# Kernel tuning notes

Measured on AMD Instinct MI355X. Metric: run time of the kernel, lower is better.

Reference implementation:

```python
import math
import jax, jax.numpy as jnp
import numpy as np

B, L, F, H = 16, 1024, 512, 8
D = F // H
FACTOR = 5.0
KEEP_MINLEN = 15.0


def setup_inputs() -> dict:
    key = jax.random.key(0)
    ks = jax.random.split(key, 12)
    inp = {
        "query": jax.random.normal(ks[0], (B, L, F), jnp.float32),
        "key": jax.random.normal(ks[1], (B, L, F), jnp.float32),
        "value": jax.random.normal(ks[2], (B, L, F), jnp.float32),
        "mask": jnp.ones((B, 1, L), jnp.int32),
    }
    s = 0.02
    inp["Wq"] = jax.random.normal(ks[3], (F, F), jnp.float32) * s
    inp["bq"] = jnp.zeros((F,), jnp.float32)
    inp["Wk"] = jax.random.normal(ks[4], (F, F), jnp.float32) * s
    inp["bk"] = jnp.zeros((F,), jnp.float32)
    inp["Wv"] = jax.random.normal(ks[5], (F, F), jnp.float32) * s
    inp["bv"] = jnp.zeros((F,), jnp.float32)
    inp["Wo"] = jax.random.normal(ks[6], (F, F), jnp.float32) * s
    inp["bo"] = jnp.zeros((F,), jnp.float32)
    return inp


def _n_top(Lq: int) -> int:
    if Lq <= KEEP_MINLEN:
        return Lq
    u = int(round(FACTOR * math.ceil(math.log(Lq))))
    return min(u, Lq)


def reference(query, key, value, mask, Wq, bq, Wk, bk, Wv, bv, Wo, bo):
    def proj(x, W, b):
        # torch nn.Linear: x @ W.T + b ; then (B,L,H,D) -> (B,H,L,D)
        return (x @ W.T + b).reshape(B, L, H, D).transpose(0, 2, 1, 3)

    q = proj(query, Wq, bq)
    k = proj(key, Wk, bk)
    v = proj(value, Wv, bv)

    # prob_QK with index=None: full (unscaled) QK to compute sparsity measure M
    scores_full = jnp.einsum('bhqd,bhkd->bhqk', q, k)  # (B,H,L,L)
    M = scores_full.max(-1) - scores_full.mean(-1)      # (B,H,L)
    u = _n_top(L)
    _, idx = jax.lax.top_k(M, u)                        # (B,H,u)

    q_red = jnp.take_along_axis(q, idx[..., None], axis=2)  # (B,H,u,D)
    scores = jnp.einsum('bhud,bhkd->bhuk', q_red, k) / math.sqrt(D)

    neg = (mask == 0)[:, None, :, :]  # (B,1,1,L) broadcasts over heads/queries
    scores = jnp.where(neg, -jnp.inf, scores)
    attn = jax.nn.softmax(scores, axis=-1)
    attn = jnp.where(neg, 0.0, attn)

    ctx_top = jnp.einsum('bhuk,bhkd->bhud', attn, v)   # (B,H,u,D)

    # initial context = mean of V over keys, broadcast to all queries
    context = jnp.broadcast_to(v.mean(axis=2, keepdims=True), (B, H, L, D))
    bi = jnp.arange(B)[:, None, None]
    hi = jnp.arange(H)[None, :, None]
    context = context.at[bi, hi, idx].set(ctx_top)

    x = context.transpose(0, 2, 1, 3).reshape(B, L, H * D)
    return x @ Wo.T + bo
```

## Files before the change

### kernel.cpp

```cpp
#include <hip/hip_runtime.h>
#include <math.h>

#define B_ 16
#define L_ 1024
#define H_ 8
#define U_ 35

typedef float f32x4 __attribute__((ext_vector_type(4)));
typedef short bf16x8 __attribute__((ext_vector_type(8)));

__device__ __forceinline__ unsigned short f2bf(float x) {
    unsigned int u = __float_as_uint(x);
    u += 0x7FFFu + ((u >> 16) & 1u);
    return (unsigned short)(u >> 16);
}
__device__ __forceinline__ float bf2f(unsigned short b) {
    return __uint_as_float(((unsigned int)b) << 16);
}

#define MFMA(a, b, c) __builtin_amdgcn_mfma_f32_16x16x32_bf16((a), (b), (c), 0, 0, 0)

#define OFF_V      ((size_t)0)
#define OFF_QHI    ((size_t)8388608)
#define OFF_QLO    ((size_t)12582912)
#define OFF_X      OFF_QHI
#define OFF_CTXP   OFF_QHI
#define OFF_KHI    ((size_t)16777216)
#define OFF_KLO    ((size_t)20971520)
#define OFF_S      ((size_t)25165824)
#define OFF_WQH    OFF_S
#define OFF_WQL    ((size_t)(OFF_S + 131072))
#define OFF_WKH    ((size_t)(OFF_S + 262144))
#define OFF_WKL    ((size_t)(OFF_S + 393216))
#define OFF_WVH    ((size_t)(OFF_S + 524288))
#define OFF_WVL    ((size_t)(OFF_S + 655360))
#define OFF_M      ((size_t)29753344)
#define OFF_KMEAN  ((size_t)29884416)
#define OFF_VMEAN  ((size_t)29892608)
#define OFF_CTX    ((size_t)29900800)
#define OFF_IDX    ((size_t)30187520)
#define OFF_WOH    ((size_t)30192000)
#define OFF_WOL    ((size_t)30323072)

__global__ __launch_bounds__(256) void split_w_kernel(
    const float* __restrict__ W, unsigned short* __restrict__ hi,
    unsigned short* __restrict__ lo)
{
    int i = blockIdx.x * 256 + threadIdx.x;
    float x = W[i];
    unsigned short h = f2bf(x);
    hi[i] = h;
    lo[i] = f2bf(x - bf2f(h));
}

__global__ __launch_bounds__(256) void gemm_mfma(
    const float* __restrict__ A,
    const unsigned short* __restrict__ Whi, const unsigned short* __restrict__ Wlo,
    const float* __restrict__ bias,
    float* __restrict__ outf,
    unsigned short* __restrict__ ohi, unsigned short* __restrict__ olo,
    const int head_layout)
{
    __shared__ unsigned short Ah[128][40];
    __shared__ unsigned short Al[128][40];
    __shared__ unsigned short Bh[128][40];
    __shared__ unsigned short Bl[128][40];
    const int tid = threadIdx.x, lane = tid & 63, wave = tid >> 6;
    const int m0 = blockIdx.x * 128, n0 = blockIdx.y * 128;
    const int wm = (wave >> 1) * 64, wn = (wave & 1) * 64;

    f32x4 zero4 = {0.f, 0.f, 0.f, 0.f};
    f32x4 acc[4][4];
#pragma unroll
    for (int i = 0; i < 4; i++)
#pragma unroll
        for (int j = 0; j < 4; j++) acc[i][j] = zero4;

    const int ar = tid >> 3, ac = (tid & 7) * 4;
    const int br = tid >> 2, bc = (tid & 3) * 8;
    const int kc = (lane >> 4) * 8;
    const int fr = lane & 15;

    for (int k0 = 0; k0 < 512; k0 += 32) {
        if (k0) __syncthreads();
#pragma unroll
        for (int p = 0; p < 4; ++p) {
            float4 a4 = *(const float4*)(A + (size_t)(m0 + ar + p * 32) * 512 + k0 + ac);
            ushort4 h4, l4;
            h4.x = f2bf(a4.x); l4.x = f2bf(a4.x - bf2f(h4.x));
            h4.y = f2bf(a4.y); l4.y = f2bf(a4.y - bf2f(h4.y));
            h4.z = f2bf(a4.z); l4.z = f2bf(a4.z - bf2f(h4.z));
            h4.w = f2bf(a4.w); l4.w = f2bf(a4.w - bf2f(h4.w));
            *(ushort4*)&Ah[ar + p * 32][ac] = h4;
            *(ushort4*)&Al[ar + p * 32][ac] = l4;
        }
#pragma unroll
        for (int p = 0; p < 2; ++p) {
            size_t off = (size_t)(n0 + br + p * 64) * 512 + k0 + bc;
            *(uint4*)&Bh[br + p * 64][bc] = *(const uint4*)(Whi + off);
            *(uint4*)&Bl[br + p * 64][bc] = *(const uint4*)(Wlo + off);
        }
        __syncthreads();

        bf16x8 ah[4], al[4];
#pragma unroll
        for (int mi = 0; mi < 4; ++mi) {
            int row = wm + mi * 16 + fr;
            ah[mi] = *(bf16x8*)&Ah[row][kc];
            al[mi] = *(bf16x8*)&Al[row][kc];
        }
#pragma unroll
        for (int ni = 0; ni < 4; ++ni) {
            int rn = wn + ni * 16 + fr;
            bf16x8 bh8 = *(bf16x8*)&Bh[rn][kc];
            bf16x8 bl8 = *(bf16x8*)&Bl[rn][kc];
#pragma unroll
            for (int mi = 0; mi < 4; ++mi) {
                acc[mi][ni] = MFMA(ah[mi], bh8, acc[mi][ni]);
                acc[mi][ni] = MFMA(ah[mi], bl8, acc[mi][ni]);
                acc[mi][ni] = MFMA(al[mi], bh8, acc[mi][ni]);
            }
        }
    }

    const int col = lane & 15, rq = (lane >> 4) * 4;
#pragma unroll
    for (int ni = 0; ni < 4; ++ni) {
        int n = n0 + wn + ni * 16 + col;
        float bn = bias[n];
#pragma unroll
        for (int mi = 0; mi < 4; ++mi) {
#pragma unroll
            for (int r = 0; r < 4; ++r) {
                int m = m0 + wm + mi * 16 + rq + r;
                float val = acc[mi][ni][r] + bn;
                if (head_layout) {
                    size_t off = ((size_t)((m >> 10) * H_ + (n >> 6)) * L_ + (m & 1023)) * 64 + (n & 63);
                    if (outf) outf[off] = val;
                    if (ohi) {
                        unsigned short h = f2bf(val);
                        ohi[off] = h;
                        olo[off] = f2bf(val - bf2f(h));
                    }
                } else {
                    outf[(size_t)m * 512 + n] = val;
                }
            }
        }
    }
}

__global__ __launch_bounds__(256) void mean_over_L(
    const float* __restrict__ src, float* __restrict__ dst)
{
    const int bh = blockIdx.x;
    const int d = threadIdx.x & 63, g = threadIdx.x >> 6;
    const float* p = src + ((size_t)bh * L_ + g * 256) * 64 + d;
    float s = 0.f;
#pragma unroll 8
    for (int l = 0; l < 256; l++) s += p[(size_t)l * 64];
    __shared__ float red[4][64];
    red[g][d] = s;
    __syncthreads();
    if (threadIdx.x < 64) {
        const int dd = threadIdx.x;
        dst[(size_t)bh * 64 + dd] =
            (red[0][dd] + red[1][dd] + red[2][dd] + red[3][dd]) * (1.0f / 1024.0f);
    }
}

__global__ __launch_bounds__(256) void mean_over_L_bf(
    const unsigned short* __restrict__ hi, const unsigned short* __restrict__ lo,
    float* __restrict__ dst)
{
    const int bh = blockIdx.x;
    const int d = threadIdx.x & 63, g = threadIdx.x >> 6;
    size_t base = ((size_t)bh * L_ + g * 256) * 64 + d;
    float s = 0.f;
#pragma unroll 8
    for (int l = 0; l < 256; l++) {
        size_t o = base + (size_t)l * 64;
        s += bf2f(hi[o]) + bf2f(lo[o]);
    }
    __shared__ float red[4][64];
    red[g][d] = s;
    __syncthreads();
    if (threadIdx.x < 64) {
        const int dd = threadIdx.x;
        dst[(size_t)bh * 64 + dd] =
            (red[0][dd] + red[1][dd] + red[2][dd] + red[3][dd]) * (1.0f / 1024.0f);
    }
}

__global__ __launch_bounds__(256) void qk_rowmax_mfma(
    const unsigned short* __restrict__ qhi, const unsigned short* __restrict__ qlo,
    const unsigned short* __restrict__ khi, const unsigned short* __restrict__ klo,
    const float* __restrict__ kmean, float* __restrict__ Mout)
{
    __shared__ unsigned short Qh[64][72], Ql[64][72];
    __shared__ unsigned short Kh[128][72], Kl[128][72];
    __shared__ float Mred[64][4];
    __shared__ float km[64];
    const int bh = blockIdx.y, q0 = blockIdx.x * 64;
    const int tid = threadIdx.x, lane = tid & 63, wave = tid >> 6;

    if (tid < 64) km[tid] = kmean[bh * 64 + tid];
    {
        int r = tid >> 2, c = (tid & 3) * 16;
        size_t off = ((size_t)bh * L_ + q0 + r) * 64 + c;
        *(uint4*)&Qh[r][c]     = *(const uint4*)(qhi + off);
        *(uint4*)&Qh[r][c + 8] = *(const uint4*)(qhi + off + 8);
        *(uint4*)&Ql[r][c]     = *(const uint4*)(qlo + off);
        *(uint4*)&Ql[r][c + 8] = *(const uint4*)(qlo + off + 8);
    }

    float rmax[4][4];
#pragma unroll
    for (int mi = 0; mi < 4; ++mi)
#pragma unroll
        for (int r = 0; r < 4; ++r) rmax[mi][r] = -INFINITY;

    const size_t kb = (size_t)bh * L_ * 64;
    const int sr = tid >> 2, sc = (tid & 3) * 16;
    const int fr = lane & 15;
    f32x4 zero4 = {0.f, 0.f, 0.f, 0.f};

    for (int kt = 0; kt < 8; ++kt) {
        __syncthreads();
        {
            size_t off = kb + (size_t)(kt * 128 + sr) * 64 + sc;
            *(uint4*)&Kh[sr][sc]          = *(const uint4*)(khi + off);
            *(uint4*)&Kh[sr][sc + 8]      = *(const uint4*)(khi + off + 8);
            *(uint4*)&Kl[sr][sc]          = *(const uint4*)(klo + off);
            *(uint4*)&Kl[sr][sc + 8]      = *(const uint4*)(klo + off + 8);
            size_t off2 = off + 64 * 64;
            *(uint4*)&Kh[sr + 64][sc]     = *(const uint4*)(khi + off2);
            *(uint4*)&Kh[sr + 64][sc + 8] = *(const uint4*)(khi + off2 + 8);
            *(uint4*)&Kl[sr + 64][sc]     = *(const uint4*)(klo + off2);
            *(uint4*)&Kl[sr + 64][sc + 8] = *(const uint4*)(klo + off2 + 8);
        }
        __syncthreads();

        f32x4 acc[4][2];
#pragma unroll
        for (int mi = 0; mi < 4; ++mi) { acc[mi][0] = zero4; acc[mi][1] = zero4; }

#pragma unroll
        for (int ks = 0; ks < 2; ++ks) {
            int kcol = ks * 32 + (lane >> 4) * 8;
            bf16x8 ah[4], al[4];
#pragma unroll
            for (int mi = 0; mi < 4; ++mi) {
                int row = mi * 16 + fr;
                ah[mi] = *(bf16x8*)&Qh[row][kcol];
                al[mi] = *(bf16x8*)&Ql[row][kcol];
            }
#pragma unroll
            for (int ni = 0; ni < 2; ++ni) {
                int krow = wave * 32 + ni * 16 + fr;
                bf16x8 bh8 = *(bf16x8*)&Kh[krow][kcol];
                bf16x8 bl8 = *(bf16x8*)&Kl[krow][kcol];
#pragma unroll
                for (int mi = 0; mi < 4; ++mi) {
                    acc[mi][ni] = MFMA(ah[mi], bh8, acc[mi][ni]);
                    acc[mi][ni] = MFMA(ah[mi], bl8, acc[mi][ni]);
                    acc[mi][ni] = MFMA(al[mi], bh8, acc[mi][ni]);
                }
            }
        }
#pragma unroll
        for (int mi = 0; mi < 4; ++mi)
#pragma unroll
            for (int r = 0; r < 4; ++r)
                rmax[mi][r] = fmaxf(rmax[mi][r], fmaxf(acc[mi][0][r], acc[mi][1][r]));
    }

#pragma unroll
    for (int mi = 0; mi < 4; ++mi)
#pragma unroll
        for (int r = 0; r < 4; ++r) {
            float v = rmax[mi][r];
            v = fmaxf(v, __shfl_xor(v, 1));
            v = fmaxf(v, __shfl_xor(v, 2));
            v = fmaxf(v, __shfl_xor(v, 4));
            v = fmaxf(v, __shfl_xor(v, 8));
            rmax[mi][r] = v;
        }
    if ((lane & 15) == 0) {
        int quad = lane >> 4;
#pragma unroll
        for (int mi = 0; mi < 4; ++mi)
#pragma unroll
            for (int r = 0; r < 4; ++r)
                Mred[mi * 16 + quad * 4 + r][wave] = rmax[mi][r];
    }
    __syncthreads();
    if (tid < 64) {
        float mx = fmaxf(fmaxf(Mred[tid][0], Mred[tid][1]),
                         fmaxf(Mred[tid][2], Mred[tid][3]));
        float dot = 0.f;
#pragma unroll 4
        for (int d = 0; d < 64; ++d)
            dot = fmaf(bf2f(Qh[tid][d]) + bf2f(Ql[tid][d]), km[d], dot);
        Mout[(size_t)bh * L_ + q0 + tid] = mx - dot;
    }
}

__global__ __launch_bounds__(256) void topk35(
    const float* __restrict__ Min, int* __restrict__ idx_out)
{
    const int bh = blockIdx.x;
    const int tid = threadIdx.x;
    __shared__ float vals[1024];
    __shared__ float wv[4];
    __shared__ int wi[4];
    for (int i = tid; i < 1024; i += 256) vals[i] = Min[(size_t)bh * 1024 + i];
    __syncthreads();
    for (int it = 0; it < U_; ++it) {
        float bv = -INFINITY; int bi = 1 << 30;
        for (int i = tid; i < 1024; i += 256) {
            float x = vals[i];
            if (x > bv) { bv = x; bi = i; }
        }
#pragma unroll
        for (int off = 32; off; off >>= 1) {
            float ov = __shfl_down(bv, off);
            int   oi = __shfl_down(bi, off);
            if (ov > bv || (ov == bv && oi < bi)) { bv = ov; bi = oi; }
        }
        if ((tid & 63) == 0) { wv[tid >> 6] = bv; wi[tid >> 6] = bi; }
        __syncthreads();
        if (tid == 0) {
#pragma unroll
            for (int w = 1; w < 4; ++w) {
                if (wv[w] > bv || (wv[w] == bv && wi[w] < bi)) { bv = wv[w]; bi = wi[w]; }
            }
            idx_out[bh * U_ + it] = bi;
            vals[bi] = -INFINITY;
        }
        __syncthreads();
    }
}

__global__ __launch_bounds__(256) void scores_red(
    const unsigned short* __restrict__ qhi, const unsigned short* __restrict__ qlo,
    const unsigned short* __restrict__ khi, const unsigned short* __restrict__ klo,
    const int* __restrict__ idx, const int* __restrict__ mask,
    float* __restrict__ S)
{
    __shared__ float Qs[64][36];
    __shared__ float Ks[64][68];
    const int bh = blockIdx.x;
    const int b = bh >> 3;
    const int tid = threadIdx.x;
    const int tk = tid & 63, tg = tid >> 6;

    for (int t = tid; t < 36 * 64; t += 256) {
        int u = t >> 6, d = t & 63;
        float val = 0.f;
        if (u < U_) {
            int l = idx[bh * U_ + u];
            size_t off = ((size_t)bh * L_ + l) * 64 + d;
            val = bf2f(qhi[off]) + bf2f(qlo[off]);
        }
        Qs[d][u] = val;
    }

    const size_t kb = (size_t)bh * L_ * 64;
    const int sr = tid >> 2, sc = (tid & 3) * 16;
    float acc[9];
    const int kt0 = blockIdx.y * 2;
    for (int ki = 0; ki < 2; ++ki) {
        int kt = kt0 + ki;
        if (ki) __syncthreads();
        {
            size_t off = kb + (size_t)(kt * 64 + sr) * 64 + sc;
            uint4 h0 = *(const uint4*)(khi + off);
            uint4 h1 = *(const uint4*)(khi + off + 8);
            uint4 l0 = *(const uint4*)(klo + off);
            uint4 l1 = *(const uint4*)(klo + off + 8);
            unsigned short hv[16], lv[16];
            *(uint4*)hv = h0; *(uint4*)(hv + 8) = h1;
            *(uint4*)lv = l0; *(uint4*)(lv + 8) = l1;
#pragma unroll
            for (int i = 0; i < 16; ++i)
                Ks[sc + i][sr] = bf2f(hv[i]) + bf2f(lv[i]);
        }
        __syncthreads();
#pragma unroll
        for (int j = 0; j < 9; j++) acc[j] = 0.f;
#pragma unroll 4
        for (int d = 0; d < 64; ++d) {
            float kv = Ks[d][tk];
#pragma unroll
            for (int j = 0; j < 9; j++) acc[j] = fmaf(Qs[d][tg + 4 * j], kv, acc[j]);
        }
        const int kcol = kt * 64 + tk;
        const bool msk = (mask[b * L_ + kcol] == 0);
#pragma unroll
        for (int j = 0; j < 9; j++) {
            int u = tg + 4 * j;
            if (u < U_)
                S[((size_t)bh * U_ + u) * 1024 + kcol] = msk ? -INFINITY : acc[j] * 0.125f;
        }
    }
}

__global__ __launch_bounds__(256) void softmax_rows(float* __restrict__ S)
{
    const size_t base = (size_t)blockIdx.x * 1024;
    const int tid = threadIdx.x;
    __shared__ float redm[4];
    __shared__ float reds[4];
    float4 v = *(const float4*)(S + base + tid * 4);
    float mx = fmaxf(fmaxf(v.x, v.y), fmaxf(v.z, v.w));
#pragma unroll
    for (int off = 32; off; off >>= 1) mx = fmaxf(mx, __shfl_down(mx, off));
    if ((tid & 63) == 0) redm[tid >> 6] = mx;
    __syncthreads();
    mx = fmaxf(fmaxf(redm[0], redm[1]), fmaxf(redm[2], redm[3]));
    float e0 = __expf(v.x - mx), e1 = __expf(v.y - mx);
    float e2 = __expf(v.z - mx), e3 = __expf(v.w - mx);
    float s = e0 + e1 + e2 + e3;
#pragma unroll
    for (int off = 32; off; off >>= 1) s += __shfl_down(s, off);
    if ((tid & 63) == 0) reds[tid >> 6] = s;
    __syncthreads();
    s = reds[0] + reds[1] + reds[2] + reds[3];
    const float inv = 1.0f / s;
    float4 o; o.x = e0 * inv; o.y = e1 * inv; o.z = e2 * inv; o.w = e3 * inv;
    *(float4*)(S + base + tid * 4) = o;
}

__global__ __launch_bounds__(256) void ctx_partial(
    const float* __restrict__ S, const float* __restrict__ v,
    float* __restrict__ ctxp)
{
    __shared__ float Vs[128][68];
    __shared__ float Wt[36][128];
    const int bh = blockIdx.x, kc = blockIdx.y;
    const int tid = threadIdx.x;
    const int td = tid & 63, tg = tid >> 6;
    const int lr = tid >> 2, lc0 = (tid & 3) * 16;

    const float* vbase = v + ((size_t)bh * L_ + kc * 128) * 64;
    const float* Sbase = S + (size_t)bh * U_ * 1024 + kc * 128;

#pragma unroll
    for (int hh = 0; hh < 2; ++hh) {
        int row = lr + hh * 64;
        const float* src = vbase + (size_t)row * 64 + lc0;
        *(float4*)&Vs[row][lc0 + 0]  = *(const float4*)(src + 0);
        *(float4*)&Vs[row][lc0 + 4]  = *(const float4*)(src + 4);
        *(float4*)&Vs[row][lc0 + 8]  = *(const float4*)(src + 8);
        *(float4*)&Vs[row][lc0 + 12] = *(const float4*)(src + 12);
    }
    for (int t = tid; t < 36 * 128; t += 256) {
        int u = t >> 7, kk = t & 127;
        Wt[u][kk] = (u < U_) ? Sbase[(size_t)u * 1024 + kk] : 0.f;
    }
    __syncthreads();

    float acc[9];
#pragma unroll
    for (int j = 0; j < 9; j++) acc[j] = 0.f;
#pragma unroll 2
    for (int kk = 0; kk < 128; ++kk) {
        float vv = Vs[kk][td];
#pragma unroll
        for (int j = 0; j < 9; j++) acc[j] = fmaf(Wt[tg + 4 * j][kk], vv, acc[j]);
    }
#pragma unroll
    for (int j = 0; j < 9; j++) {
        int u = tg + 4 * j;
        if (u < U_)
            ctxp[((size_t)(kc * 128 + bh) * 36 + u) * 64 + td] = acc[j];
    }
}

__global__ __launch_bounds__(256) void ctx_reduce(
    const float* __restrict__ ctxp, float* __restrict__ ctx)
{
    const int i = blockIdx.x * 256 + threadIdx.x;
    const int d = i & 63;
    const int rest = i >> 6;
    const int u = rest % U_;
    const int bh = rest / U_;
    float s = 0.f;
#pragma unroll
    for (int kc = 0; kc < 8; ++kc)
        s += ctxp[((size_t)(kc * 128 + bh) * 36 + u) * 64 + d];
    ctx[i] = s;
}

__global__ void fill_x_kernel(const float* __restrict__ vmean, float* __restrict__ x)
{
    const size_t i = (size_t)blockIdx.x * 256 + threadIdx.x;
    const int n = (int)(i & 511);
    const int b = (int)(i >> 19);
    x[i] = vmean[((b << 3) + (n >> 6)) * 64 + (n & 63)];
}

__global__ void scatter_ctx_kernel(const float* __restrict__ ctx, const int* __restrict__ idx,
                                   float* __restrict__ x)
{
    const int r = blockIdx.x;
    const int bh = r / U_;
    const int b = bh >> 3, h = bh & 7;
    const int l = idx[r];
    x[(((size_t)b * L_ + l) << 9) + (h << 6) + threadIdx.x] = ctx[(size_t)r * 64 + threadIdx.x];
}

extern "C" void kernel_launch(void* const* d_in, const int* in_sizes, int n_in,
                              void* d_out, int out_size, void* d_ws, size_t ws_size,
                              hipStream_t stream)
{
    (void)in_sizes; (void)n_in; (void)out_size; (void)ws_size;
    const float* query = (const float*)d_in[0];
    const float* key   = (const float*)d_in[1];
    const float* value = (const float*)d_in[2];
    const int*   mask  = (const int*)d_in[3];
    const float* Wq = (const float*)d_in[4];
    const float* bq = (const float*)d_in[5];
    const float* Wk = (const float*)d_in[6];
    const float* bk = (const float*)d_in[7];
    const float* Wv = (const float*)d_in[8];
    const float* bvp = (const float*)d_in[9];
    const float* Wo = (const float*)d_in[10];
    const float* bo = (const float*)d_in[11];
    float* out = (float*)d_out;

    float* ws = (float*)d_ws;
    float* v      = ws + OFF_V;
    unsigned short* q_hi = (unsigned short*)(ws + OFF_QHI);
    unsigned short* q_lo = (unsigned short*)(ws + OFF_QLO);
    unsigned short* k_hi = (unsigned short*)(ws + OFF_KHI);
    unsigned short* k_lo = (unsigned short*)(ws + OFF_KLO);
    float* x      = ws + OFF_X;
    float* ctxp   = ws + OFF_CTXP;
    float* S      = ws + OFF_S;
    float* Marr   = ws + OFF_M;
    float* kmean  = ws + OFF_KMEAN;
    float* vmean  = ws + OFF_VMEAN;
    float* ctx    = ws + OFF_CTX;
    int*   idx    = (int*)(ws + OFF_IDX);
    unsigned short* wqh = (unsigned short*)(ws + OFF_WQH);
    unsigned short* wql = (unsigned short*)(ws + OFF_WQL);
    unsigned short* wkh = (unsigned short*)(ws + OFF_WKH);
    unsigned short* wkl = (unsigned short*)(ws + OFF_WKL);
    unsigned short* wvh = (unsigned short*)(ws + OFF_WVH);
    unsigned short* wvl = (unsigned short*)(ws + OFF_WVL);
    unsigned short* woh = (unsigned short*)(ws + OFF_WOH);
    unsigned short* wol = (unsigned short*)(ws + OFF_WOL);

    split_w_kernel<<<1024, 256, 0, stream>>>(Wq, wqh, wql);
    split_w_kernel<<<1024, 256, 0, stream>>>(Wk, wkh, wkl);
    split_w_kernel<<<1024, 256, 0, stream>>>(Wv, wvh, wvl);
    split_w_kernel<<<1024, 256, 0, stream>>>(Wo, woh, wol);

    const dim3 ggemm(128, 4);
    gemm_mfma<<<ggemm, 256, 0, stream>>>(query, wqh, wql, bq, nullptr, q_hi, q_lo, 1);
    gemm_mfma<<<ggemm, 256, 0, stream>>>(key,   wkh, wkl, bk, nullptr, k_hi, k_lo, 1);
    gemm_mfma<<<ggemm, 256, 0, stream>>>(value, wvh, wvl, bvp, v, nullptr, nullptr, 1);

    mean_over_L_bf<<<128, 256, 0, stream>>>(k_hi, k_lo, kmean);
    mean_over_L<<<128, 256, 0, stream>>>(v, vmean);

    qk_rowmax_mfma<<<dim3(16, 128), 256, 0, stream>>>(q_hi, q_lo, k_hi, k_lo, kmean, Marr);
    topk35<<<128, 256, 0, stream>>>(Marr, idx);

    scores_red<<<dim3(128, 8), 256, 0, stream>>>(q_hi, q_lo, k_hi, k_lo, idx, mask, S);
    softmax_rows<<<B_ * H_ * U_, 256, 0, stream>>>(S);
    ctx_partial<<<dim3(128, 8), 256, 0, stream>>>(S, v, ctxp);
    ctx_reduce<<<1120, 256, 0, stream>>>(ctxp, ctx);

    fill_x_kernel<<<32768, 256, 0, stream>>>(vmean, x);
    scatter_ctx_kernel<<<B_ * H_ * U_, 64, 0, stream>>>(ctx, idx, x);
    gemm_mfma<<<ggemm, 256, 0, stream>>>(x, woh, wol, bo, out, nullptr, nullptr, 0);
}
```

Before: 510.4 us.

## Replace output GEMM with broadcast of projected V-mean plus sparse delta updates

Most rows of the context equal the per-head V mean, so the output is computed as a per-batch projected mean broadcast to every row. Only the selected top-u rows receive a correction (ctx minus mean) times Wo, added with atomics. This removes the full L×F×F output GEMM, the x fill/scatter kernels and the Wo split. The change also merges the weight-split and mean kernels into single launches and register-prefetches the next K tile in qk_rowmax. It adds atomics and changes fp32 summation order on the output path.

After: 513.0 us. No clear change (+0.5%).

```diff
diff --git a/kernel.cpp b/kernel.cpp
--- a/kernel.cpp
+++ b/kernel.cpp
@@ -23,7 +23,6 @@
 #define OFF_V      ((size_t)0)
 #define OFF_QHI    ((size_t)8388608)
 #define OFF_QLO    ((size_t)12582912)
-#define OFF_X      OFF_QHI
 #define OFF_CTXP   OFF_QHI
 #define OFF_KHI    ((size_t)16777216)
 #define OFF_KLO    ((size_t)20971520)
@@ -37,16 +36,22 @@
 #define OFF_M      ((size_t)29753344)
 #define OFF_KMEAN  ((size_t)29884416)
 #define OFF_VMEAN  ((size_t)29892608)
-#define OFF_CTX    ((size_t)29900800)
+#define OFF_CTXD   ((size_t)29900800)
 #define OFF_IDX    ((size_t)30187520)
-#define OFF_WOH    ((size_t)30192000)
-#define OFF_WOL    ((size_t)30323072)
-
-__global__ __launch_bounds__(256) void split_w_kernel(
-    const float* __restrict__ W, unsigned short* __restrict__ hi,
-    unsigned short* __restrict__ lo)
-{
-    int i = blockIdx.x * 256 + threadIdx.x;
+#define OFF_OBASE  ((size_t)30192000)
+
+__global__ __launch_bounds__(256) void split_w3(
+    const float* __restrict__ Wq, const float* __restrict__ Wk,
+    const float* __restrict__ Wv,
+    unsigned short* __restrict__ wqh, unsigned short* __restrict__ wql,
+    unsigned short* __restrict__ wkh, unsigned short* __restrict__ wkl,
+    unsigned short* __restrict__ wvh, unsigned short* __restrict__ wvl)
+{
+    const int w = blockIdx.x >> 10;
+    const int i = (blockIdx.x & 1023) * 256 + threadIdx.x;
+    const float* W = (w == 0) ? Wq : (w == 1) ? Wk : Wv;
+    unsigned short* hi = (w == 0) ? wqh : (w == 1) ? wkh : wvh;
+    unsigned short* lo = (w == 0) ? wql : (w == 1) ? wkl : wvl;
     float x = W[i];
     unsigned short h = f2bf(x);
     hi[i] = h;
@@ -150,45 +155,33 @@
     }
 }
 
-__global__ __launch_bounds__(256) void mean_over_L(
-    const float* __restrict__ src, float* __restrict__ dst)
-{
-    const int bh = blockIdx.x;
+__global__ __launch_bounds__(256) void means_fused(
+    const unsigned short* __restrict__ khi, const unsigned short* __restrict__ klo,
+    const float* __restrict__ v, float* __restrict__ kmean, float* __restrict__ vmean)
+{
+    const int which = blockIdx.x >> 7;
+    const int bh = blockIdx.x & 127;
     const int d = threadIdx.x & 63, g = threadIdx.x >> 6;
-    const float* p = src + ((size_t)bh * L_ + g * 256) * 64 + d;
+    __shared__ float red[4][64];
     float s = 0.f;
+    if (which == 0) {
+        size_t base = ((size_t)bh * L_ + g * 256) * 64 + d;
 #pragma unroll 8
-    for (int l = 0; l < 256; l++) s += p[(size_t)l * 64];
-    __shared__ float red[4][64];
+        for (int l = 0; l < 256; l++) {
+            size_t o = base + (size_t)l * 64;
+            s += bf2f(khi[o]) + bf2f(klo[o]);
+        }
+    } else {
+        const float* p = v + ((size_t)bh * L_ + g * 256) * 64 + d;
+#pragma unroll 8
+        for (int l = 0; l < 256; l++) s += p[(size_t)l * 64];
+    }
     red[g][d] = s;
     __syncthreads();
     if (threadIdx.x < 64) {
         const int dd = threadIdx.x;
-        dst[(size_t)bh * 64 + dd] =
-            (red[0][dd] + red[1][dd] + red[2][dd] + red[3][dd]) * (1.0f / 1024.0f);
-    }
-}
-
-__global__ __launch_bounds__(256) void mean_over_L_bf(
-    const unsigned short* __restrict__ hi, const unsigned short* __restrict__ lo,
-    float* __restrict__ dst)
-{
-    const int bh = blockIdx.x;
-    const int d = threadIdx.x & 63, g = threadIdx.x >> 6;
-    size_t base = ((size_t)bh * L_ + g * 256) * 64 + d;
-    float s = 0.f;
-#pragma unroll 8
-    for (int l = 0; l < 256; l++) {
-        size_t o = base + (size_t)l * 64;
-        s += bf2f(hi[o]) + bf2f(lo[o]);
-    }
-    __shared__ float red[4][64];
-    red[g][d] = s;
-    __syncthreads();
-    if (threadIdx.x < 64) {
-        const int dd = threadIdx.x;
-        dst[(size_t)bh * 64 + dd] =
-            (red[0][dd] + red[1][dd] + red[2][dd] + red[3][dd]) * (1.0f / 1024.0f);
+        float m = (red[0][dd] + red[1][dd] + red[2][dd] + red[3][dd]) * (1.0f / 1024.0f);
+        (which == 0 ? kmean : vmean)[(size_t)bh * 64 + dd] = m;
     }
 }
 
@@ -225,21 +218,32 @@
     const int fr = lane & 15;
     f32x4 zero4 = {0.f, 0.f, 0.f, 0.f};
 
+    uint4 ph0a, ph0b, pl0a, pl0b, ph1a, ph1b, pl1a, pl1b;
+    {
+        size_t off = kb + (size_t)sr * 64 + sc;
+        ph0a = *(const uint4*)(khi + off);       ph0b = *(const uint4*)(khi + off + 8);
+        pl0a = *(const uint4*)(klo + off);       pl0b = *(const uint4*)(klo + off + 8);
+        size_t off2 = off + 4096;
+        ph1a = *(const uint4*)(khi + off2);      ph1b = *(const uint4*)(khi + off2 + 8);
+        pl1a = *(const uint4*)(klo + off2);      pl1b = *(const uint4*)(klo + off2 + 8);
+    }
+
     for (int kt = 0; kt < 8; ++kt) {
         __syncthreads();
-        {
-            size_t off = kb + (size_t)(kt * 128 + sr) * 64 + sc;
-            *(uint4*)&Kh[sr][sc]          = *(const uint4*)(khi + off);
-            *(uint4*)&Kh[sr][sc + 8]      = *(const uint4*)(khi + off + 8);
-            *(uint4*)&Kl[sr][sc]          = *(const uint4*)(klo + off);
-            *(uint4*)&Kl[sr][sc + 8]      = *(const uint4*)(klo + off + 8);
-            size_t off2 = off + 64 * 64;
-            *(uint4*)&Kh[sr + 64][sc]     = *(const uint4*)(khi + off2);
-            *(uint4*)&Kh[sr + 64][sc + 8] = *(const uint4*)(khi + off2 + 8);
-            *(uint4*)&Kl[sr + 64][sc]     = *(const uint4*)(klo + off2);
-            *(uint4*)&Kl[sr + 64][sc + 8] = *(const uint4*)(klo + off2 + 8);
-        }
+        *(uint4*)&Kh[sr][sc]          = ph0a;  *(uint4*)&Kh[sr][sc + 8]      = ph0b;
+        *(uint4*)&Kl[sr][sc]          = pl0a;  *(uint4*)&Kl[sr][sc + 8]      = pl0b;
+        *(uint4*)&Kh[sr + 64][sc]     = ph1a;  *(uint4*)&Kh[sr + 64][sc + 8] = ph1b;
+        *(uint4*)&Kl[sr + 64][sc]     = pl1a;  *(uint4*)&Kl[sr + 64][sc + 8] = pl1b;
         __syncthreads();
+
+        if (kt < 7) {
+            size_t off = kb + (size_t)((kt + 1) * 128 + sr) * 64 + sc;
+            ph0a = *(const uint4*)(khi + off);       ph0b = *(const uint4*)(khi + off + 8);
+            pl0a = *(const uint4*)(klo + off);       pl0b = *(const uint4*)(klo + off + 8);
+            size_t off2 = off + 4096;
+            ph1a = *(const uint4*)(khi + off2);      ph1b = *(const uint4*)(khi + off2 + 8);
+            pl1a = *(const uint4*)(klo + off2);      pl1b = *(const uint4*)(klo + off2 + 8);
+        }
 
         f32x4 acc[4][2];
 #pragma unroll
@@ -478,8 +482,9 @@
     }
 }
 
-__global__ __launch_bounds__(256) void ctx_reduce(
-    const float* __restrict__ ctxp, float* __restrict__ ctx)
+__global__ __launch_bounds__(256) void ctx_reduce_diff(
+    const float* __restrict__ ctxp, const float* __restrict__ vmean,
+    float* __restrict__ ctxd)
 {
     const int i = blockIdx.x * 256 + threadIdx.x;
     const int d = i & 63;
@@ -490,25 +495,72 @@
 #pragma unroll
     for (int kc = 0; kc < 8; ++kc)
         s += ctxp[((size_t)(kc * 128 + bh) * 36 + u) * 64 + d];
-    ctx[i] = s;
-}
-
-__global__ void fill_x_kernel(const float* __restrict__ vmean, float* __restrict__ x)
-{
-    const size_t i = (size_t)blockIdx.x * 256 + threadIdx.x;
-    const int n = (int)(i & 511);
-    const int b = (int)(i >> 19);
-    x[i] = vmean[((b << 3) + (n >> 6)) * 64 + (n & 63)];
-}
-
-__global__ void scatter_ctx_kernel(const float* __restrict__ ctx, const int* __restrict__ idx,
-                                   float* __restrict__ x)
-{
-    const int r = blockIdx.x;
-    const int bh = r / U_;
-    const int b = bh >> 3, h = bh & 7;
-    const int l = idx[r];
-    x[(((size_t)b * L_ + l) << 9) + (h << 6) + threadIdx.x] = ctx[(size_t)r * 64 + threadIdx.x];
+    ctxd[i] = s - vmean[(size_t)bh * 64 + d];
+}
+
+__global__ __launch_bounds__(256) void vmean_proj(
+    const float* __restrict__ vmean, const float* __restrict__ Wo,
+    const float* __restrict__ bo, float* __restrict__ obase)
+{
+    const int b = blockIdx.x >> 3, n0 = (blockIdx.x & 7) * 64;
+    const int tid = threadIdx.x;
+    __shared__ float xbar[512];
+    __shared__ float psum[64][5];
+    for (int i = tid; i < 512; i += 256)
+        xbar[i] = vmean[(size_t)(b * 8 + (i >> 6)) * 64 + (i & 63)];
+    __syncthreads();
+    const int n = n0 + (tid >> 2), fq = (tid & 3) * 128;
+    float s = 0.f;
+    for (int f = 0; f < 128; f += 4) {
+        float4 w = *(const float4*)(Wo + (size_t)n * 512 + fq + f);
+        s += xbar[fq + f] * w.x + xbar[fq + f + 1] * w.y +
+             xbar[fq + f + 2] * w.z + xbar[fq + f + 3] * w.w;
+    }
+    psum[tid >> 2][tid & 3] = s;
+    __syncthreads();
+    if (tid < 64)
+        obase[(size_t)b * 512 + n0 + tid] =
+            psum[tid][0] + psum[tid][1] + psum[tid][2] + psum[tid][3] + bo[n0 + tid];
+}
+
+__global__ void broadcast_out(const float* __restrict__ obase, float* __restrict__ out)
+{
+    const size_t e = ((size_t)blockIdx.x * 256 + threadIdx.x) * 4;
+    const int n = (int)(e & 511);
+    const int b = (int)(e >> 19);
+    *(float4*)(out + e) = *(const float4*)(obase + (b << 9) + n);
+}
+
+__global__ __launch_bounds__(256) void delta_out(
+    const float* __restrict__ ctxd, const int* __restrict__ idx,
+    const float* __restrict__ Wo, float* __restrict__ out)
+{
+    const int bh = blockIdx.x, b = bh >> 3, h = bh & 7;
+    const int tid = threadIdx.x;
+    __shared__ int ls[U_];
+    if (tid < U_) ls[tid] = idx[bh * U_ + tid];
+    __syncthreads();
+    const float* dbase = ctxd + (size_t)bh * U_ * 64;
+    const float* w0p = Wo + (size_t)tid * 512 + h * 64;
+    const float* w1p = w0p + (size_t)256 * 512;
+    float acc0[U_], acc1[U_];
+#pragma unroll
+    for (int u = 0; u < U_; ++u) { acc0[u] = 0.f; acc1[u] = 0.f; }
+    for (int jc = 0; jc < 16; ++jc) {
+        float4 w0 = *(const float4*)(w0p + jc * 4);
+        float4 w1 = *(const float4*)(w1p + jc * 4);
+#pragma unroll
+        for (int u = 0; u < U_; ++u) {
+            float4 dv = *(const float4*)(dbase + u * 64 + jc * 4);
+            acc0[u] = fmaf(dv.w, w0.w, fmaf(dv.z, w0.z, fmaf(dv.y, w0.y, fmaf(dv.x, w0.x, acc0[u]))));
+            acc1[u] = fmaf(dv.w, w1.w, fmaf(dv.z, w1.z, fmaf(dv.y, w1.y, fmaf(dv.x, w1.x, acc1[u]))));
+        }
+    }
+    for (int u = 0; u < U_; ++u) {
+        float* orow = out + ((size_t)b * L_ + ls[u]) * 512;
+        atomicAdd(orow + tid, acc0[u]);
+        atomicAdd(orow + tid + 256, acc1[u]);
+    }
 }
 
 extern "C" void kernel_launch(void* const* d_in, const int* in_sizes, int n_in,
@@ -536,35 +588,30 @@
     unsigned short* q_lo = (unsigned short*)(ws + OFF_QLO);
     unsigned short* k_hi = (unsigned short*)(ws + OFF_KHI);
     unsigned short* k_lo = (unsigned short*)(ws + OFF_KLO);
-    float* x      = ws + OFF_X;
     float* ctxp   = ws + OFF_CTXP;
     float* S      = ws + OFF_S;
     float* Marr   = ws + OFF_M;
     float* kmean  = ws + OFF_KMEAN;
     float* vmean  = ws + OFF_VMEAN;
-    float* ctx    = ws + OFF_CTX;
+    float* ctxd   = ws + OFF_CTXD;
     int*   idx    = (int*)(ws + OFF_IDX);
+    float* obase  = ws + OFF_OBASE;
     unsigned short* wqh = (unsigned short*)(ws + OFF_WQH);
     unsigned short* wql = (unsigned short*)(ws + OFF_WQL);
     unsigned short* wkh = (unsigned short*)(ws + OFF_WKH);
     unsigned short* wkl = (unsigned short*)(ws + OFF_WKL);
     unsigned short* wvh = (unsigned short*)(ws + OFF_WVH);
     unsigned short* wvl = (unsigned short*)(ws + OFF_WVL);
-    unsigned short* woh = (unsigned short*)(ws + OFF_WOH);
-    unsigned short* wol = (unsigned short*)(ws + OFF_WOL);
-
-    split_w_kernel<<<1024, 256, 0, stream>>>(Wq, wqh, wql);
-    split_w_kernel<<<1024, 256, 0, stream>>>(Wk, wkh, wkl);
-    split_w_kernel<<<1024, 256, 0, stream>>>(Wv, wvh, wvl);
-    split_w_kernel<<<1024, 256, 0, stream>>>(Wo, woh, wol);
+
+    split_w3<<<3072, 256, 0, stream>>>(Wq, Wk, Wv, wqh, wql, wkh, wkl, wvh, wvl);
 
     const dim3 ggemm(128, 4);
     gemm_mfma<<<ggemm, 256, 0, stream>>>(query, wqh, wql, bq, nullptr, q_hi, q_lo, 1);
     gemm_mfma<<<ggemm, 256, 0, stream>>>(key,   wkh, wkl, bk, nullptr, k_hi, k_lo, 1);
     gemm_mfma<<<ggemm, 256, 0, stream>>>(value, wvh, wvl, bvp, v, nullptr, nullptr, 1);
 
-    mean_over_L_bf<<<128, 256, 0, stream>>>(k_hi, k_lo, kmean);
-    mean_over_L<<<128, 256, 0, stream>>>(v, vmean);
+    means_fused<<<256, 256, 0, stream>>>(k_hi, k_lo, v, kmean, vmean);
+    vmean_proj<<<128, 256, 0, stream>>>(vmean, Wo, bo, obase);
 
     qk_rowmax_mfma<<<dim3(16, 128), 256, 0, stream>>>(q_hi, q_lo, k_hi, k_lo, kmean, Marr);
     topk35<<<128, 256, 0, stream>>>(Marr, idx);
@@ -572,9 +619,8 @@
     scores_red<<<dim3(128, 8), 256, 0, stream>>>(q_hi, q_lo, k_hi, k_lo, idx, mask, S);
     softmax_rows<<<B_ * H_ * U_, 256, 0, stream>>>(S);
     ctx_partial<<<dim3(128, 8), 256, 0, stream>>>(S, v, ctxp);
-    ctx_reduce<<<1120, 256, 0, stream>>>(ctxp, ctx);
-
-    fill_x_kernel<<<32768, 256, 0, stream>>>(vmean, x);
-    scatter_ctx_kernel<<<B_ * H_ * U_, 64, 0, stream>>>(ctx, idx, x);
-    gemm_mfma<<<ggemm, 256, 0, stream>>>(x, woh, wol, bo, out, nullptr, nullptr, 0);
-}
+    ctx_reduce_diff<<<1120, 256, 0, stream>>>(ctxp, vmean, ctxd);
+
+    broadcast_out<<<8192, 256, 0, stream>>>(obase, out);
+    delta_out<<<128, 256, 0, stream>>>(ctxd, idx, Wo, out);
+}
```
